# Optimization experiments

Hardware: AMD Instinct MI355X
Metric: run time of the kernel (lower is better)

The kernel has to match this reference:

```python
import jax, jax.numpy as jnp
import numpy as np

N = 100000      # nodes
E = 1600000     # edges
G = 1000        # graphs in the batch
D_IN, D_H, D_OUT = 128, 128, 64


def setup_inputs() -> dict:
    key = jax.random.key(0)
    ks = jax.random.split(key, 8)
    x = jax.random.normal(ks[0], (N, D_IN), jnp.float32)
    edge_index = jax.random.randint(ks[1], (2, E), 0, N, dtype=jnp.int32)
    batch = jnp.sort(jax.random.randint(ks[2], (N,), 0, G, dtype=jnp.int32))
    s_in = 1.0 / np.sqrt(D_IN)
    s_h = 1.0 / np.sqrt(D_H)
    return {
        "x": x,
        "edge_index": edge_index,
        "batch": batch,
        "W_emb": jax.random.normal(ks[3], (D_IN, D_H), jnp.float32) * s_in,
        "b_emb": jnp.zeros((D_H,), jnp.float32),
        "W1": jax.random.normal(ks[4], (D_H, D_H), jnp.float32) * s_h,
        "b1": jnp.zeros((D_H,), jnp.float32),
        "W2": jax.random.normal(ks[5], (D_H, D_H), jnp.float32) * s_h,
        "b2": jnp.zeros((D_H,), jnp.float32),
        "W3": jax.random.normal(ks[6], (D_H, D_OUT), jnp.float32) * s_h,
        "b3": jnp.zeros((D_OUT,), jnp.float32),
    }


def reference(x, edge_index, batch, W_emb, b_emb, W1, b1, W2, b2, W3, b3):
    # Eval mode: dropout is identity.
    n = x.shape[0]
    src, dst = edge_index[0], edge_index[1]
    # GCN symmetric normalization with self-loops (Kipf & Welling).
    deg = jax.ops.segment_sum(jnp.ones(src.shape[0], x.dtype), dst, num_segments=n) + 1.0
    dis = jax.lax.rsqrt(deg)                 # deg^{-1/2}, [N]
    edge_norm = dis[src] * dis[dst]          # [E]
    self_norm = dis * dis                    # self-loop weight = 1/deg, [N]

    def gcn_conv(h, W, b):
        h = h @ W                                         # [N, d_out]
        agg = jax.ops.segment_sum(h[src] * edge_norm[:, None], dst, num_segments=n)
        return agg + h * self_norm[:, None] + b

    h = x @ W_emb + b_emb
    h = jax.nn.relu(gcn_conv(h, W1, b1))
    h = jax.nn.relu(gcn_conv(h, W2, b2))
    h = gcn_conv(h, W3, b3)
    # global_add_pool over graph ids
    return jax.ops.segment_sum(h, batch, num_segments=G)
```

## Files before the change

### kernel.cpp

```cpp
#include <hip/hip_runtime.h>
#include <hip/hip_bf16.h>

#define NN 100000
#define NE 1600000
#define NG 1000
#define SMAX 48

typedef unsigned short u16;
typedef unsigned int u32;
typedef u16 u16x8 __attribute__((ext_vector_type(8)));
typedef u32 u32x4 __attribute__((ext_vector_type(4)));
typedef float f32x4 __attribute__((ext_vector_type(4)));
typedef __attribute__((ext_vector_type(8))) short s16x8;
typedef __attribute__((ext_vector_type(4))) float facc4;

__device__ __forceinline__ float bf2f(u16 u) {
    union { u32 i; float f; } c; c.i = ((u32)u) << 16; return c.f;
}
__device__ __forceinline__ u16 f2bf(float f) {
    __hip_bfloat16 h = __float2bfloat16(f);
    union { __hip_bfloat16 h; u16 u; } c; c.h = h; return c.u;
}
__device__ __forceinline__ int ntload(const int* p) { return __builtin_nontemporal_load(p); }

__global__ __launch_bounds__(256) void detect_kernel(const u32* __restrict__ xr, int* __restrict__ flag) {
    __shared__ int cnt[256];
    int c = 0;
    for (int i = threadIdx.x; i < 4096; i += 256) {
        u32 e = (xr[i] >> 7) & 0xFFu;
        if (e >= 110u && e <= 135u) c++;
    }
    cnt[threadIdx.x] = c;
    __syncthreads();
    for (int o = 128; o > 0; o >>= 1) {
        if (threadIdx.x < o) cnt[threadIdx.x] += cnt[threadIdx.x + o];
        __syncthreads();
    }
    if (threadIdx.x == 0) flag[0] = (cnt[0] > 2048) ? 1 : 0;
}

#define MEGA_NB 12726
__global__ __launch_bounds__(256) void mega_prep(
    const void* __restrict__ x, const int* __restrict__ flag, u16* __restrict__ xb,
    const void* __restrict__ Wemb, const void* __restrict__ W1, const void* __restrict__ W2,
    const void* __restrict__ W3, u16* __restrict__ wembT, u16* __restrict__ w1T,
    u16* __restrict__ w2T, u16* __restrict__ w3T,
    const void* __restrict__ bemb, const void* __restrict__ b1, const void* __restrict__ b2,
    const void* __restrict__ b3, float* __restrict__ bembF, float* __restrict__ b1F,
    float* __restrict__ b2F, float* __restrict__ b3F,
    const int* __restrict__ ei, int* __restrict__ counts)
{
    int b = blockIdx.x, tid = threadIdx.x;
    int fl = flag[0];
    if (b < 6250) {
        if (fl) return;
        int c = b * 256 + tid;
        f32x4 a = reinterpret_cast<const f32x4*>(x)[c * 2];
        f32x4 d = reinterpret_cast<const f32x4*>(x)[c * 2 + 1];
        u16x8 o;
        #pragma unroll
        for (int j = 0; j < 4; ++j) { o[j] = f2bf(a[j]); o[4 + j] = f2bf(d[j]); }
        reinterpret_cast<u16x8*>(xb)[c] = o;
    } else if (b < 6474) {
        int o = (b - 6250) * 256 + tid;
        const void* src; u16* dst; int M; int ol;
        if (o < 16384)      { src = Wemb; dst = wembT; M = 128; ol = o; }
        else if (o < 32768) { src = W1;   dst = w1T;   M = 128; ol = o - 16384; }
        else if (o < 49152) { src = W2;   dst = w2T;   M = 128; ol = o - 32768; }
        else                { src = W3;   dst = w3T;   M = 64;  ol = o - 49152; }
        int n = ol >> 7, k = ol & 127;
        u16 v = fl ? reinterpret_cast<const u16*>(src)[k * M + n]
                   : f2bf(reinterpret_cast<const float*>(src)[k * M + n]);
        dst[ol] = v;
    } else if (b < 6476) {
        int i = (b - 6474) * 256 + tid;
        if (i >= 448) return;
        const void* src; float* dst; int il;
        if (i < 128)      { src = bemb; dst = bembF; il = i; }
        else if (i < 256) { src = b1;   dst = b1F;   il = i - 128; }
        else if (i < 384) { src = b2;   dst = b2F;   il = i - 256; }
        else              { src = b3;   dst = b3F;   il = i - 384; }
        dst[il] = fl ? bf2f(reinterpret_cast<const u16*>(src)[il])
                     : reinterpret_cast<const float*>(src)[il];
    } else {
        int e = (b - 6476) * 256 + tid;
        if (e < NE) atomicAdd(&counts[ei[NE + e]], 1);
    }
}

__global__ __launch_bounds__(256) void scan1_kernel(const int* __restrict__ counts, int* __restrict__ offs,
                                                    int* __restrict__ bsums, float* __restrict__ dis,
                                                    int* __restrict__ cursor) {
    __shared__ int sums[256];
    int tid = threadIdx.x;
    int base = blockIdx.x * 2048 + tid * 8;
    int local[8];
    int s = 0;
    #pragma unroll
    for (int i = 0; i < 8; ++i) {
        int v = 0;
        if (base + i < NN) {
            v = counts[base + i];
            dis[base + i] = rsqrtf((float)v + 1.0f);
            cursor[base + i] = 0;
        }
        local[i] = s; s += v;
    }
    sums[tid] = s;
    __syncthreads();
    for (int o = 1; o < 256; o <<= 1) {
        int v = (tid >= o) ? sums[tid - o] : 0;
        __syncthreads();
        sums[tid] += v;
        __syncthreads();
    }
    int excl = sums[tid] - s;
    #pragma unroll
    for (int i = 0; i < 8; ++i)
        if (base + i < NN) offs[base + i] = excl + local[i];
    if (tid == 255) bsums[blockIdx.x] = sums[255];
}

__global__ __launch_bounds__(256) void scan3_kernel(int* __restrict__ offs, const int* __restrict__ bsums) {
    __shared__ int addv;
    int i = blockIdx.x * 256 + threadIdx.x;
    int bucket = blockIdx.x >> 3;
    if (threadIdx.x == 0) {
        int s = 0;
        for (int k = 0; k < bucket; ++k) s += bsums[k];
        addv = s;
    }
    __syncthreads();
    if (i < NN) offs[i] += addv;
}

__global__ __launch_bounds__(256) void mega2_kernel(
    const u16* __restrict__ Hin, const u16* __restrict__ HinAlt, const int* __restrict__ flag,
    const u16* __restrict__ Wt, const float* __restrict__ bias, u16* __restrict__ Hout,
    const int* __restrict__ ei, const int* __restrict__ offs, int* __restrict__ cursor,
    int* __restrict__ srcs)
{
    __shared__ u16 sW[128 * 136];
    int b = blockIdx.x, tid = threadIdx.x;
    if (b < 1563) {
        const u16* A = flag[0] ? HinAlt : Hin;
        for (int c = tid; c < 128 * 16; c += 256) {
            int n = c >> 4, kc = (c & 15) << 3;
            *reinterpret_cast<u16x8*>(sW + n * 136 + kc) = reinterpret_cast<const u16x8*>(Wt)[c];
        }
        __syncthreads();
        int wv = tid >> 6, lane = tid & 63;
        int m = lane & 15, quad = lane >> 4;
        int r0 = b * 64 + wv * 16;
        int ar = r0 + m; if (ar >= NN) ar = NN - 1;
        facc4 acc[8];
        #pragma unroll
        for (int t = 0; t < 8; ++t) acc[t] = (facc4){0.f, 0.f, 0.f, 0.f};
        const u16* arow = A + (size_t)ar * 128 + quad * 8;
        #pragma unroll
        for (int k0 = 0; k0 < 128; k0 += 32) {
            s16x8 a = *reinterpret_cast<const s16x8*>(arow + k0);
            #pragma unroll
            for (int t = 0; t < 8; ++t) {
                s16x8 bfr = *reinterpret_cast<const s16x8*>(sW + (t * 16 + m) * 136 + k0 + quad * 8);
                acc[t] = __builtin_amdgcn_mfma_f32_16x16x32_bf16(a, bfr, acc[t], 0, 0, 0);
            }
        }
        #pragma unroll
        for (int t = 0; t < 8; ++t) {
            int col = t * 16 + m;
            float bv = bias[col];
            #pragma unroll
            for (int r = 0; r < 4; ++r) {
                int orow = r0 + quad * 4 + r;
                if (orow < NN)
                    Hout[(size_t)orow * 128 + col] = f2bf(acc[t][r] + bv);
            }
        }
    } else {
        int e = (b - 1563) * 256 + tid;
        if (e < NE) {
            int s = ei[e], d = ei[NE + e];
            int pos = offs[d] + atomicAdd(&cursor[d], 1);
            srcs[pos] = s;
        }
    }
}

__global__ __launch_bounds__(256) void gemm_mfma128(const u16* __restrict__ Hin, const u16* __restrict__ Wt,
                                                    u16* __restrict__ Hout) {
    __shared__ u16 sW[128 * 136];
    int tid = threadIdx.x;
    for (int c = tid; c < 128 * 16; c += 256) {
        int n = c >> 4, kc = (c & 15) << 3;
        *reinterpret_cast<u16x8*>(sW + n * 136 + kc) = reinterpret_cast<const u16x8*>(Wt)[c];
    }
    __syncthreads();
    int wv = tid >> 6, lane = tid & 63;
    int m = lane & 15, quad = lane >> 4;
    int r0 = blockIdx.x * 64 + wv * 16;
    int ar = r0 + m; if (ar >= NN) ar = NN - 1;
    facc4 acc[8];
    #pragma unroll
    for (int t = 0; t < 8; ++t) acc[t] = (facc4){0.f, 0.f, 0.f, 0.f};
    const u16* arow = Hin + (size_t)ar * 128 + quad * 8;
    #pragma unroll
    for (int k0 = 0; k0 < 128; k0 += 32) {
        s16x8 a = *reinterpret_cast<const s16x8*>(arow + k0);
        #pragma unroll
        for (int t = 0; t < 8; ++t) {
            s16x8 bfr = *reinterpret_cast<const s16x8*>(sW + (t * 16 + m) * 136 + k0 + quad * 8);
            acc[t] = __builtin_amdgcn_mfma_f32_16x16x32_bf16(a, bfr, acc[t], 0, 0, 0);
        }
    }
    #pragma unroll
    for (int t = 0; t < 8; ++t) {
        int col = t * 16 + m;
        #pragma unroll
        for (int r = 0; r < 4; ++r) {
            int orow = r0 + quad * 4 + r;
            if (orow < NN)
                Hout[(size_t)orow * 128 + col] = f2bf(acc[t][r]);
        }
    }
}

template <int MOUT>
__global__ __launch_bounds__(256) void fused_agg_gemm(const u16* __restrict__ T, const int* __restrict__ offs,
                                                      const int* __restrict__ counts, const float* __restrict__ dis,
                                                      const int* __restrict__ srcs, const float* __restrict__ aggbias,
                                                      const u16* __restrict__ Wt, u16* __restrict__ Hout) {
    constexpr int LDW = 136;
    __shared__ u16 sW[MOUT * LDW];
    __shared__ u16 sA[64 * LDW];
    int tid = threadIdx.x;
    for (int c = tid; c < MOUT * 16; c += 256) {
        int n = c >> 4, kc = (c & 15) << 3;
        *reinterpret_cast<u16x8*>(sW + n * LDW + kc) = reinterpret_cast<const u16x8*>(Wt)[c];
    }

    int lane = tid & 15, grp = tid >> 4;
    const u32x4* T4 = reinterpret_cast<const u32x4*>(T);
    for (int i = 0; i < 4; ++i) {
        int nl = grp * 4 + i;
        int n = blockIdx.x * 64 + nl;
        bool valid = n < NN;
        int nc = valid ? n : NN - 1;
        float di = dis[nc];
        float sn = di * di;
        u32x4 ts = T4[(size_t)nc * 16 + lane];
        float acc[8];
        #pragma unroll
        for (int q = 0; q < 4; ++q) {
            acc[2 * q]     = bf2f((u16)(ts[q] & 0xffffu)) * sn + aggbias[lane * 8 + 2 * q];
            acc[2 * q + 1] = bf2f((u16)(ts[q] >> 16))     * sn + aggbias[lane * 8 + 2 * q + 1];
        }
        int st = offs[nc], cnt = valid ? counts[nc] : 0;
        int j = 0;
        for (; j + 4 <= cnt; j += 4) {
            int e0 = ntload(srcs + st + j);
            int e1 = ntload(srcs + st + j + 1);
            int e2 = ntload(srcs + st + j + 2);
            int e3 = ntload(srcs + st + j + 3);
            float w0 = dis[e0] * di, w1 = dis[e1] * di, w2 = dis[e2] * di, w3 = dis[e3] * di;
            u32x4 g0 = T4[(size_t)e0 * 16 + lane];
            u32x4 g1 = T4[(size_t)e1 * 16 + lane];
            u32x4 g2 = T4[(size_t)e2 * 16 + lane];
            u32x4 g3 = T4[(size_t)e3 * 16 + lane];
            #pragma unroll
            for (int q = 0; q < 4; ++q) {
                acc[2 * q]     += bf2f((u16)(g0[q] & 0xffffu)) * w0;
                acc[2 * q + 1] += bf2f((u16)(g0[q] >> 16))     * w0;
                acc[2 * q]     += bf2f((u16)(g1[q] & 0xffffu)) * w1;
                acc[2 * q + 1] += bf2f((u16)(g1[q] >> 16))     * w1;
                acc[2 * q]     += bf2f((u16)(g2[q] & 0xffffu)) * w2;
                acc[2 * q + 1] += bf2f((u16)(g2[q] >> 16))     * w2;
                acc[2 * q]     += bf2f((u16)(g3[q] & 0xffffu)) * w3;
                acc[2 * q + 1] += bf2f((u16)(g3[q] >> 16))     * w3;
            }
        }
        for (; j < cnt; ++j) {
            int e = ntload(srcs + st + j);
            float w = dis[e] * di;
            u32x4 g = T4[(size_t)e * 16 + lane];
            #pragma unroll
            for (int q = 0; q < 4; ++q) {
                acc[2 * q]     += bf2f((u16)(g[q] & 0xffffu)) * w;
                acc[2 * q + 1] += bf2f((u16)(g[q] >> 16))     * w;
            }
        }
        u16x8 pk;
        #pragma unroll
        for (int q = 0; q < 4; ++q) {
            pk[2 * q]     = f2bf(fmaxf(acc[2 * q], 0.0f));
            pk[2 * q + 1] = f2bf(fmaxf(acc[2 * q + 1], 0.0f));
        }
        *reinterpret_cast<u16x8*>(sA + nl * LDW + lane * 8) = pk;
    }
    __syncthreads();

    int wv = tid >> 6, l64 = tid & 63;
    int m = l64 & 15, quad = l64 >> 4;
    int r0 = blockIdx.x * 64 + wv * 16;
    constexpr int NT = MOUT / 16;
    facc4 gacc[NT];
    #pragma unroll
    for (int t = 0; t < NT; ++t) gacc[t] = (facc4){0.f, 0.f, 0.f, 0.f};
    #pragma unroll
    for (int k0 = 0; k0 < 128; k0 += 32) {
        s16x8 a = *reinterpret_cast<const s16x8*>(sA + (wv * 16 + m) * LDW + k0 + quad * 8);
        #pragma unroll
        for (int t = 0; t < NT; ++t) {
            s16x8 bfr = *reinterpret_cast<const s16x8*>(sW + (t * 16 + m) * LDW + k0 + quad * 8);
            gacc[t] = __builtin_amdgcn_mfma_f32_16x16x32_bf16(a, bfr, gacc[t], 0, 0, 0);
        }
    }
    #pragma unroll
    for (int t = 0; t < NT; ++t) {
        int col = t * 16 + m;
        #pragma unroll
        for (int r = 0; r < 4; ++r) {
            int orow = r0 + quad * 4 + r;
            if (orow < NN)
                Hout[(size_t)orow * MOUT + col] = f2bf(gacc[t][r]);
        }
    }
}

__global__ __launch_bounds__(256) void agg_pool_kernel(const u16* __restrict__ T, const int* __restrict__ offs,
                                                       const int* __restrict__ counts, const float* __restrict__ dis,
                                                       const int* __restrict__ srcs, const float* __restrict__ bias,
                                                       const int* __restrict__ batch, float* __restrict__ outF) {
    __shared__ float accG[SMAX * 64];
    __shared__ int sg0;
    int tid = threadIdx.x;
    for (int i = tid; i < SMAX * 64; i += 256) accG[i] = 0.0f;
    if (tid == 0) sg0 = batch[blockIdx.x * 32];
    __syncthreads();
    int g0 = sg0;
    int lane = tid & 7;
    int n = blockIdx.x * 32 + (tid >> 3);

    const u32x4* T4 = reinterpret_cast<const u32x4*>(T);
    float di = dis[n];
    float sn = di * di;
    u32x4 ts = T4[(size_t)n * 8 + lane];
    float acc[8];
    #pragma unroll
    for (int q = 0; q < 4; ++q) {
        acc[2 * q]     = bf2f((u16)(ts[q] & 0xffffu)) * sn + bias[lane * 8 + 2 * q];
        acc[2 * q + 1] = bf2f((u16)(ts[q] >> 16))     * sn + bias[lane * 8 + 2 * q + 1];
    }
    int st = offs[n], cnt = counts[n];
    int j = 0;
    for (; j + 4 <= cnt; j += 4) {
        int e0 = ntload(srcs + st + j);
        int e1 = ntload(srcs + st + j + 1);
        int e2 = ntload(srcs + st + j + 2);
        int e3 = ntload(srcs + st + j + 3);
        float w0 = dis[e0] * di, w1 = dis[e1] * di, w2 = dis[e2] * di, w3 = dis[e3] * di;
        u32x4 g0v = T4[(size_t)e0 * 8 + lane];
        u32x4 g1v = T4[(size_t)e1 * 8 + lane];
        u32x4 g2v = T4[(size_t)e2 * 8 + lane];
        u32x4 g3v = T4[(size_t)e3 * 8 + lane];
        #pragma unroll
        for (int q = 0; q < 4; ++q) {
            acc[2 * q]     += bf2f((u16)(g0v[q] & 0xffffu)) * w0;
            acc[2 * q + 1] += bf2f((u16)(g0v[q] >> 16))     * w0;
            acc[2 * q]     += bf2f((u16)(g1v[q] & 0xffffu)) * w1;
            acc[2 * q + 1] += bf2f((u16)(g1v[q] >> 16))     * w1;
            acc[2 * q]     += bf2f((u16)(g2v[q] & 0xffffu)) * w2;
            acc[2 * q + 1] += bf2f((u16)(g2v[q] >> 16))     * w2;
            acc[2 * q]     += bf2f((u16)(g3v[q] & 0xffffu)) * w3;
            acc[2 * q + 1] += bf2f((u16)(g3v[q] >> 16))     * w3;
        }
    }
    for (; j < cnt; ++j) {
        int e = ntload(srcs + st + j);
        float w = dis[e] * di;
        u32x4 g = T4[(size_t)e * 8 + lane];
        #pragma unroll
        for (int q = 0; q < 4; ++q) {
            acc[2 * q]     += bf2f((u16)(g[q] & 0xffffu)) * w;
            acc[2 * q + 1] += bf2f((u16)(g[q] >> 16))     * w;
        }
    }

    int s = batch[n] - g0;
    if (s >= 0 && s < SMAX) {
        #pragma unroll
        for (int q = 0; q < 8; ++q)
            atomicAdd(&accG[s * 64 + lane * 8 + q], acc[q]);
    } else {
        #pragma unroll
        for (int q = 0; q < 8; ++q)
            atomicAdd(&outF[(size_t)(g0 + s) * 64 + lane * 8 + q], acc[q]);
    }
    __syncthreads();
    int gend = batch[blockIdx.x * 32 + 31];
    int span = gend - g0 + 1;
    if (span > SMAX) span = SMAX;
    for (int i = tid; i < span * 64; i += 256)
        atomicAdd(&outF[(size_t)g0 * 64 + i], accG[i]);
}

__global__ __launch_bounds__(256) void out_cvt_kernel(const float* __restrict__ outF, void* __restrict__ out,
                                                      const int* __restrict__ flag) {
    int i = blockIdx.x * 256 + threadIdx.x;
    if (i < NG * 64) {
        float v = outF[i];
        if (flag[0]) reinterpret_cast<u16*>(out)[i] = f2bf(v);
        else         reinterpret_cast<float*>(out)[i] = v;
    }
}

extern "C" void kernel_launch(void* const* d_in, const int* in_sizes, int n_in,
                              void* d_out, int out_size, void* d_ws, size_t ws_size,
                              hipStream_t stream) {
    const void* x     = d_in[0];
    const int* ei     = (const int*)d_in[1];
    const int* batch  = (const int*)d_in[2];
    const void* W_emb = d_in[3];
    const void* b_emb = d_in[4];
    const void* W1    = d_in[5];
    const void* b1    = d_in[6];
    const void* W2    = d_in[7];
    const void* b2    = d_in[8];
    const void* W3    = d_in[9];
    const void* b3    = d_in[10];

    char* p = (char*)d_ws;
    auto alloc = [&](size_t bytes) { void* r = p; p += (bytes + 255) & ~(size_t)255; return r; };
    int*   flag   = (int*)alloc(256);
    int*   counts = (int*)alloc(NN * 4);
    int*   cursor = (int*)alloc(NN * 4);
    int*   offs   = (int*)alloc(NN * 4);
    float* dis    = (float*)alloc(NN * 4);
    int*   bsums  = (int*)alloc(256 * 4);
    int*   srcs   = (int*)alloc((size_t)NE * 4);
    u16*   wembT  = (u16*)alloc(128 * 128 * 2);
    u16*   w1T    = (u16*)alloc(128 * 128 * 2);
    u16*   w2T    = (u16*)alloc(128 * 128 * 2);
    u16*   w3T    = (u16*)alloc(64 * 128 * 2);
    float* bembF  = (float*)alloc(128 * 4);
    float* b1F    = (float*)alloc(128 * 4);
    float* b2F    = (float*)alloc(128 * 4);
    float* b3F    = (float*)alloc(64 * 4);
    float* outF   = (float*)alloc((size_t)NG * 64 * 4);
    u16*   hA     = (u16*)alloc((size_t)(NN + 64) * 128 * 2);
    u16*   hB     = (u16*)alloc((size_t)(NN + 64) * 128 * 2);

    hipMemsetAsync(counts, 0, NN * 4, stream);
    hipMemsetAsync(outF, 0, (size_t)NG * 64 * 4, stream);

    const int SB = (NN + 2047) / 2048;
    const int NB = (NN + 255) / 256;
    const int GB = (NN + 63) / 64;

    detect_kernel<<<1, 256, 0, stream>>>((const u32*)x, flag);
    mega_prep<<<MEGA_NB, 256, 0, stream>>>(x, flag, hB, W_emb, W1, W2, W3, wembT, w1T, w2T, w3T,
                                           b_emb, b1, b2, b3, bembF, b1F, b2F, b3F, ei, counts);
    scan1_kernel<<<SB, 256, 0, stream>>>(counts, offs, bsums, dis, cursor);
    scan3_kernel<<<NB, 256, 0, stream>>>(offs, bsums);

    mega2_kernel<<<GB + (NE + 255) / 256, 256, 0, stream>>>(hB, (const u16*)x, flag, wembT, bembF, hA,
                                                            ei, offs, cursor, srcs);
    gemm_mfma128<<<GB, 256, 0, stream>>>(hA, w1T, hB);
    fused_agg_gemm<128><<<GB, 256, 0, stream>>>(hB, offs, counts, dis, srcs, b1F, w2T, hA);
    fused_agg_gemm<64><<<GB, 256, 0, stream>>>(hA, offs, counts, dis, srcs, b2F, w3T, hB);
    agg_pool_kernel<<<NN / 32, 256, 0, stream>>>(hB, offs, counts, dis, srcs, b3F, batch, outF);
    out_cvt_kernel<<<(NG * 64 + 255) / 256, 256, 0, stream>>>(outF, d_out, flag);
}
```

Before: 577.2 us.

## Fold embedding into first GCN weight, removing one full-size GEMM pass

Precomputes a fused weight W_emb·W1 and bias b_emb·W1 in a small kernel, so the first node-level transform becomes a single GEMM on x instead of two back-to-back GEMMs. This removes the separate gemm_mfma128 pass over all nodes, along with one write and one read of the full hidden matrix. The edge-scatter blocks are also reordered to come first in the combined kernel, and B fragments are now read directly from global memory instead of being staged in LDS. The fused weight is rounded to bf16 once, which changes numerics slightly.

```diff
diff --git a/kernel.cpp b/kernel.cpp
--- a/kernel.cpp
+++ b/kernel.cpp
@@ -88,6 +88,29 @@
     }
 }
 
+__global__ __launch_bounds__(256) void wfuse_kernel(const u16* __restrict__ w1T, const u16* __restrict__ wembT,
+                                                    const float* __restrict__ bembF,
+                                                    u16* __restrict__ WfT, float* __restrict__ bfW) {
+    int b = blockIdx.x;
+    if (b < 64) {
+        int o = b * 256 + threadIdx.x;
+        int n = o >> 7, k = o & 127;
+        float acc = 0.f;
+        #pragma unroll 4
+        for (int j = 0; j < 128; ++j)
+            acc += bf2f(w1T[n * 128 + j]) * bf2f(wembT[j * 128 + k]);
+        WfT[o] = f2bf(acc);
+    } else {
+        int n = threadIdx.x;
+        if (n < 128) {
+            float acc = 0.f;
+            for (int j = 0; j < 128; ++j)
+                acc += bembF[j] * bf2f(w1T[n * 128 + j]);
+            bfW[n] = acc;
+        }
+    }
+}
+
 __global__ __launch_bounds__(256) void scan1_kernel(const int* __restrict__ counts, int* __restrict__ offs,
                                                     int* __restrict__ bsums, float* __restrict__ dis,
                                                     int* __restrict__ cursor) {
@@ -134,24 +157,27 @@
     if (i < NN) offs[i] += addv;
 }
 
-__global__ __launch_bounds__(256) void mega2_kernel(
-    const u16* __restrict__ Hin, const u16* __restrict__ HinAlt, const int* __restrict__ flag,
-    const u16* __restrict__ Wt, const float* __restrict__ bias, u16* __restrict__ Hout,
+#define MEGA2_SCAT 6250
+__global__ __launch_bounds__(256, 5) void mega2_kernel(
+    const u16* __restrict__ xb, const u16* __restrict__ xraw, const int* __restrict__ flag,
+    const u16* __restrict__ WfT, const float* __restrict__ bfW, u16* __restrict__ Hout,
     const int* __restrict__ ei, const int* __restrict__ offs, int* __restrict__ cursor,
     int* __restrict__ srcs)
 {
-    __shared__ u16 sW[128 * 136];
     int b = blockIdx.x, tid = threadIdx.x;
-    if (b < 1563) {
-        const u16* A = flag[0] ? HinAlt : Hin;
-        for (int c = tid; c < 128 * 16; c += 256) {
-            int n = c >> 4, kc = (c & 15) << 3;
-            *reinterpret_cast<u16x8*>(sW + n * 136 + kc) = reinterpret_cast<const u16x8*>(Wt)[c];
-        }
-        __syncthreads();
+    if (b < MEGA2_SCAT) {
+        int e = b * 256 + tid;
+        if (e < NE) {
+            int s = ei[e], d = ei[NE + e];
+            int pos = offs[d] + atomicAdd(&cursor[d], 1);
+            srcs[pos] = s;
+        }
+    } else {
+        const u16* A = flag[0] ? xraw : xb;
+        int gb = b - MEGA2_SCAT;
         int wv = tid >> 6, lane = tid & 63;
         int m = lane & 15, quad = lane >> 4;
-        int r0 = b * 64 + wv * 16;
+        int r0 = gb * 64 + wv * 16;
         int ar = r0 + m; if (ar >= NN) ar = NN - 1;
         facc4 acc[8];
         #pragma unroll
@@ -162,65 +188,20 @@
             s16x8 a = *reinterpret_cast<const s16x8*>(arow + k0);
             #pragma unroll
             for (int t = 0; t < 8; ++t) {
-                s16x8 bfr = *reinterpret_cast<const s16x8*>(sW + (t * 16 + m) * 136 + k0 + quad * 8);
+                s16x8 bfr = *reinterpret_cast<const s16x8*>(WfT + (t * 16 + m) * 128 + k0 + quad * 8);
                 acc[t] = __builtin_amdgcn_mfma_f32_16x16x32_bf16(a, bfr, acc[t], 0, 0, 0);
             }
         }
         #pragma unroll
         for (int t = 0; t < 8; ++t) {
             int col = t * 16 + m;
-            float bv = bias[col];
+            float bv = bfW[col];
             #pragma unroll
             for (int r = 0; r < 4; ++r) {
                 int orow = r0 + quad * 4 + r;
                 if (orow < NN)
                     Hout[(size_t)orow * 128 + col] = f2bf(acc[t][r] + bv);
             }
-        }
-    } else {
-        int e = (b - 1563) * 256 + tid;
-        if (e < NE) {
-            int s = ei[e], d = ei[NE + e];
-            int pos = offs[d] + atomicAdd(&cursor[d], 1);
-            srcs[pos] = s;
-        }
-    }
-}
-
-__global__ __launch_bounds__(256) void gemm_mfma128(const u16* __restrict__ Hin, const u16* __restrict__ Wt,
-                                                    u16* __restrict__ Hout) {
-    __shared__ u16 sW[128 * 136];
-    int tid = threadIdx.x;
-    for (int c = tid; c < 128 * 16; c += 256) {
-        int n = c >> 4, kc = (c & 15) << 3;
-        *reinterpret_cast<u16x8*>(sW + n * 136 + kc) = reinterpret_cast<const u16x8*>(Wt)[c];
-    }
-    __syncthreads();
-    int wv = tid >> 6, lane = tid & 63;
-    int m = lane & 15, quad = lane >> 4;
-    int r0 = blockIdx.x * 64 + wv * 16;
-    int ar = r0 + m; if (ar >= NN) ar = NN - 1;
-    facc4 acc[8];
-    #pragma unroll
-    for (int t = 0; t < 8; ++t) acc[t] = (facc4){0.f, 0.f, 0.f, 0.f};
-    const u16* arow = Hin + (size_t)ar * 128 + quad * 8;
-    #pragma unroll
-    for (int k0 = 0; k0 < 128; k0 += 32) {
-        s16x8 a = *reinterpret_cast<const s16x8*>(arow + k0);
-        #pragma unroll
-        for (int t = 0; t < 8; ++t) {
-            s16x8 bfr = *reinterpret_cast<const s16x8*>(sW + (t * 16 + m) * 136 + k0 + quad * 8);
-            acc[t] = __builtin_amdgcn_mfma_f32_16x16x32_bf16(a, bfr, acc[t], 0, 0, 0);
-        }
-    }
-    #pragma unroll
-    for (int t = 0; t < 8; ++t) {
-        int col = t * 16 + m;
-        #pragma unroll
-        for (int r = 0; r < 4; ++r) {
-            int orow = r0 + quad * 4 + r;
-            if (orow < NN)
-                Hout[(size_t)orow * 128 + col] = f2bf(acc[t][r]);
         }
     }
 }
@@ -442,10 +423,12 @@
     u16*   w1T    = (u16*)alloc(128 * 128 * 2);
     u16*   w2T    = (u16*)alloc(128 * 128 * 2);
     u16*   w3T    = (u16*)alloc(64 * 128 * 2);
+    u16*   WfT    = (u16*)alloc(128 * 128 * 2);
     float* bembF  = (float*)alloc(128 * 4);
     float* b1F    = (float*)alloc(128 * 4);
     float* b2F    = (float*)alloc(128 * 4);
     float* b3F    = (float*)alloc(64 * 4);
+    float* bfW    = (float*)alloc(128 * 4);
     float* outF   = (float*)alloc((size_t)NG * 64 * 4);
     u16*   hA     = (u16*)alloc((size_t)(NN + 64) * 128 * 2);
     u16*   hB     = (u16*)alloc((size_t)(NN + 64) * 128 * 2);
@@ -460,14 +443,14 @@
     detect_kernel<<<1, 256, 0, stream>>>((const u32*)x, flag);
     mega_prep<<<MEGA_NB, 256, 0, stream>>>(x, flag, hB, W_emb, W1, W2, W3, wembT, w1T, w2T, w3T,
                                            b_emb, b1, b2, b3, bembF, b1F, b2F, b3F, ei, counts);
+    wfuse_kernel<<<65, 256, 0, stream>>>(w1T, wembT, bembF, WfT, bfW);
     scan1_kernel<<<SB, 256, 0, stream>>>(counts, offs, bsums, dis, cursor);
     scan3_kernel<<<NB, 256, 0, stream>>>(offs, bsums);
 
-    mega2_kernel<<<GB + (NE + 255) / 256, 256, 0, stream>>>(hB, (const u16*)x, flag, wembT, bembF, hA,
-                                                            ei, offs, cursor, srcs);
-    gemm_mfma128<<<GB, 256, 0, stream>>>(hA, w1T, hB);
-    fused_agg_gemm<128><<<GB, 256, 0, stream>>>(hB, offs, counts, dis, srcs, b1F, w2T, hA);
-    fused_agg_gemm<64><<<GB, 256, 0, stream>>>(hA, offs, counts, dis, srcs, b2F, w3T, hB);
-    agg_pool_kernel<<<NN / 32, 256, 0, stream>>>(hB, offs, counts, dis, srcs, b3F, batch, outF);
+    mega2_kernel<<<MEGA2_SCAT + GB, 256, 0, stream>>>(hB, (const u16*)x, flag, WfT, bfW, hA,
+                                                      ei, offs, cursor, srcs);
+    fused_agg_gemm<128><<<GB, 256, 0, stream>>>(hA, offs, counts, dis, srcs, b1F, w2T, hB);
+    fused_agg_gemm<64><<<GB, 256, 0, stream>>>(hB, offs, counts, dis, srcs, b2F, w3T, hA);
+    agg_pool_kernel<<<NN / 32, 256, 0, stream>>>(hA, offs, counts, dis, srcs, b3F, batch, outF);
     out_cvt_kernel<<<(NG * 64 + 255) / 256, 256, 0, stream>>>(outF, d_out, flag);
 }
```

Measured after the change: 582.0 us. About the same (+0.8%).
